# Performance work log

Hardware: AMD Instinct MI355X
Metric: run time of the kernel (lower is better)

The kernel has to match this reference:

```python
import jax, jax.numpy as jnp
import numpy as np

N_NODES = 50000
N_EDGES = 600000
N_GRAPHS = 64
IN_D, HID, EMB = 5, 128, 64
BN_EPS = 1e-5


def setup_inputs() -> dict:
    key = jax.random.key(0)
    ks = jax.random.split(key, 16)
    x = jax.random.normal(ks[0], (N_NODES, IN_D), dtype=jnp.float32)
    src = jax.random.randint(ks[1], (N_EDGES,), 0, N_NODES, dtype=jnp.int32)
    dst = jax.random.randint(ks[2], (N_EDGES,), 0, N_NODES, dtype=jnp.int32)
    batch = jnp.sort(jax.random.randint(ks[3], (N_NODES,), 0, N_GRAPHS, dtype=jnp.int32))
    def lin(k, fi, fo):
        s = 1.0 / np.sqrt(fi)
        kw, kb = jax.random.split(k)
        return (jax.random.uniform(kw, (fi, fo), jnp.float32, -s, s),
                jax.random.uniform(kb, (fo,), jnp.float32, -s, s))
    W1, b1 = lin(ks[4], IN_D, HID)
    W2, b2 = lin(ks[5], HID, HID)
    W3, b3 = lin(ks[6], HID, HID)
    Wp, bp = lin(ks[7], HID, EMB)
    g1 = 1.0 + 0.1 * jax.random.normal(ks[8], (HID,), jnp.float32)
    g2 = 1.0 + 0.1 * jax.random.normal(ks[9], (HID,), jnp.float32)
    g3 = 1.0 + 0.1 * jax.random.normal(ks[10], (HID,), jnp.float32)
    be1 = 0.1 * jax.random.normal(ks[11], (HID,), jnp.float32)
    be2 = 0.1 * jax.random.normal(ks[12], (HID,), jnp.float32)
    be3 = 0.1 * jax.random.normal(ks[13], (HID,), jnp.float32)
    return dict(x=x, src=src, dst=dst, batch=batch,
                W1=W1, b1=b1, W2=W2, b2=b2, W3=W3, b3=b3,
                g1=g1, be1=be1, g2=g2, be2=be2, g3=g3, be3=be3,
                Wp=Wp, bp=bp)


def reference(x, src, dst, batch, W1, b1, W2, b2, W3, b3,
              g1, be1, g2, be2, g3, be3, Wp, bp):
    n = x.shape[0]
    # GCNConv with self-loops and symmetric normalization (PyG default)
    loop = jnp.arange(n, dtype=src.dtype)
    s = jnp.concatenate([src, loop])
    d = jnp.concatenate([dst, loop])
    deg = jax.ops.segment_sum(jnp.ones_like(d, dtype=x.dtype), d, num_segments=n)
    dinv = jnp.where(deg > 0, jax.lax.rsqrt(deg), 0.0)
    norm = (dinv[s] * dinv[d])[:, None]  # (E+N, 1)

    def gcn(h, W, b):
        hw = h @ W                                   # (N, HID)
        msg = hw[s] * norm                           # gather + scale
        agg = jax.ops.segment_sum(msg, d, num_segments=n)
        return agg + b

    def bn_relu(h, g, be):
        # eval-mode BatchNorm1d with running_mean=0, running_var=1
        return jax.nn.relu(h * (g * jax.lax.rsqrt(jnp.asarray(1.0 + BN_EPS, h.dtype))) + be)

    h = bn_relu(gcn(x, W1, b1), g1, be1)
    h = bn_relu(gcn(h, W2, b2), g2, be2)
    h = bn_relu(gcn(h, W3, b3), g3, be3)

    # global mean pool over graphs
    sums = jax.ops.segment_sum(h, batch, num_segments=N_GRAPHS)
    cnt = jax.ops.segment_sum(jnp.ones((n,), h.dtype), batch, num_segments=N_GRAPHS)
    pooled = sums / jnp.maximum(cnt, 1.0)[:, None]
    return pooled @ Wp + bp
```

## Files before the change

kernel.cpp:

```cpp
#include <hip/hip_runtime.h>
#include <hip/hip_fp16.h>

#define N_NODES 50000
#define N_EDGES 600000
#define N_GRAPHS 64
#define IN_D 5
#define HID 128
#define EMB 64

#define CHUNK 512
#define NCHUNK ((N_NODES + CHUNK - 1) / CHUNK)
#define NREP 16
#define NLOC 4
#define TB 16

typedef _Float16 half8 __attribute__((ext_vector_type(8)));
typedef float float4v __attribute__((ext_vector_type(4)));
typedef float floatx2 __attribute__((ext_vector_type(2)));

__device__ __forceinline__ float ep_w(unsigned pe) {
    return (float)__ushort_as_half((unsigned short)(pe >> 16));
}
__device__ __forceinline__ unsigned ep_s(unsigned pe) { return pe & 0xffffu; }


__global__ __launch_bounds__(256) void k_init(int* __restrict__ cnt) {
    int tid = blockIdx.x * blockDim.x + threadIdx.x;
    if (tid < N_NODES) cnt[tid] = 0;
}


__global__ __launch_bounds__(256) void k_count(
        const int* __restrict__ dst, int* __restrict__ cnt,
        float* __restrict__ psum_rep,
        const float* __restrict__ W2, const float* __restrict__ W3,
        _Float16* __restrict__ Wt2, _Float16* __restrict__ Wt3,
        unsigned int* __restrict__ e_pack,
        const float* __restrict__ x, float* __restrict__ xp) {
    int tid = blockIdx.x * blockDim.x + threadIdx.x;
    int nt = gridDim.x * blockDim.x;
    if (tid < N_EDGES) atomicAdd(&cnt[dst[tid]], 1);
    if (tid < 8) e_pack[N_EDGES + tid] = 0u;
    for (int i = tid; i < NREP * N_GRAPHS * HID; i += nt) psum_rep[i] = 0.f;
    for (int i = tid; i < N_NODES * 8; i += nt) {
        int f = i & 7, n = i >> 3;
        xp[i] = (f < IN_D) ? x[n * IN_D + f] : 0.f;
    }
    for (int i = tid; i < 2 * HID * HID; i += nt) {
        int rem = i & (HID * HID - 1);
        int k = rem & 127, f = rem >> 7;
        if (i < HID * HID) Wt2[rem] = (_Float16)W2[k * HID + f];
        else               Wt3[rem] = (_Float16)W3[k * HID + f];
    }
}


__global__ void k_chunksum(const int* __restrict__ cnt, int* __restrict__ csum,
                           float* __restrict__ dinv) {
    __shared__ int sh[256];
    int b = blockIdx.x, t = threadIdx.x;
    int i0 = b * CHUNK + t, i1 = i0 + 256;
    int v = 0;
    if (i0 < N_NODES) { int c = cnt[i0]; v += c; dinv[i0] = rsqrtf((float)c + 1.0f); }
    if (i1 < N_NODES) { int c = cnt[i1]; v += c; dinv[i1] = rsqrtf((float)c + 1.0f); }
    sh[t] = v; __syncthreads();
    for (int off = 128; off > 0; off >>= 1) {
        if (t < off) sh[t] += sh[t + off];
        __syncthreads();
    }
    if (t == 0) csum[b] = sh[0];
}


__global__ void k_scan(const int* __restrict__ cnt, const int* __restrict__ csum,
                       int* __restrict__ row_start) {
    __shared__ int ws[4];
    int b = blockIdx.x, t = threadIdx.x;
    int lane = t & 63, w = t >> 6;

    int pre = 0;
    for (int j = lane; j < b; j += 64) pre += csum[j];
    #pragma unroll
    for (int off = 32; off > 0; off >>= 1) pre += __shfl_down(pre, off);
    pre = __shfl(pre, 0);

    int base = b * CHUNK;
    int i0 = base + 2 * t, i1 = i0 + 1;
    int c0 = (i0 < N_NODES) ? cnt[i0] : 0;
    int c1 = (i1 < N_NODES) ? cnt[i1] : 0;
    int v = c0 + c1;
    int s = v;
    #pragma unroll
    for (int off = 1; off < 64; off <<= 1) {
        int u = __shfl_up(s, off);
        if (lane >= off) s += u;
    }
    if (lane == 63) ws[w] = s;
    __syncthreads();
    if (t == 0) {
        int r = 0;
        #pragma unroll
        for (int j = 0; j < 4; ++j) { int xx = ws[j]; ws[j] = r; r += xx; }
    }
    __syncthreads();
    int excl = s - v + ws[w] + pre;
    if (i0 < N_NODES) row_start[i0] = excl;
    if (i1 < N_NODES) row_start[i1] = excl + c0;
    if (b == 0 && t == 0) row_start[N_NODES] = N_EDGES;
}


__global__ __launch_bounds__(256) void k_scatter(
        const int* __restrict__ src, const int* __restrict__ dst,
        const float* __restrict__ dinv, const int* __restrict__ row_start,
        int* __restrict__ cnt, unsigned int* __restrict__ e_pack) {
    int e = blockIdx.x * blockDim.x + threadIdx.x;
    if (e >= N_EDGES) return;
    int d = dst[e];
    int pos = row_start[d] + atomicSub(&cnt[d], 1) - 1;
    int s = src[e];
    unsigned hw = (unsigned)__half_as_ushort(__float2half(dinv[s]));
    e_pack[pos] = (hw << 16) | (unsigned)s;
}


__global__ __launch_bounds__(256) void k_agg1(
        const float* __restrict__ xp, const float* __restrict__ dinv,
        const int* __restrict__ row_start, const unsigned int* __restrict__ e_pack,
        const float* __restrict__ W1, const float* __restrict__ b1,
        const float* __restrict__ g1, const float* __restrict__ be1,
        unsigned short* __restrict__ H8u) {
    int t = threadIdx.x;
    int w = t >> 6, lane = t & 63;
    int slot8 = lane >> 3, q8 = lane & 7;
    int nb = blockIdx.x * TB;

    const float rs = rsqrtf(1.0f + 1e-5f);
    int fa = lane * 2, fb = fa + 1;
    float w1a[IN_D], w1b[IN_D];
    #pragma unroll
    for (int k = 0; k < IN_D; ++k) {
        w1a[k] = W1[k * HID + fa];
        w1b[k] = W1[k * HID + fb];
    }
    float b1a = b1[fa], b1b = b1[fb];
    float g1a = g1[fa] * rs, g1b = g1[fb] * rs;
    float e1a = be1[fa], e1b = be1[fb];

    #pragma unroll 1
    for (int i = 0; i < 2; ++i) {
        int n0 = nb + w * 4 + i * 2;
        int beg0 = row_start[n0], end0 = row_start[n0 + 1], end1 = row_start[n0 + 2];
        float acc0 = 0.f, acc1 = 0.f;
        int e0 = beg0, e1 = end0;
        while (e0 < end0 && e1 < end1) {
            unsigned pe0 = e_pack[e0 + slot8];
            unsigned pe1 = e_pack[e1 + slot8];
            float fw0 = (e0 + slot8 < end0) ? ep_w(pe0) : 0.f;
            float fw1 = (e1 + slot8 < end1) ? ep_w(pe1) : 0.f;
            float v0 = xp[(size_t)ep_s(pe0) * 8 + q8];
            float v1 = xp[(size_t)ep_s(pe1) * 8 + q8];
            acc0 = fmaf(fw0, v0, acc0);
            acc1 = fmaf(fw1, v1, acc1);
            e0 += 8; e1 += 8;
        }
        while (e0 < end0) {
            unsigned pe0 = e_pack[e0 + slot8];
            float fw0 = (e0 + slot8 < end0) ? ep_w(pe0) : 0.f;
            acc0 = fmaf(fw0, xp[(size_t)ep_s(pe0) * 8 + q8], acc0);
            e0 += 8;
        }
        while (e1 < end1) {
            unsigned pe1 = e_pack[e1 + slot8];
            float fw1 = (e1 + slot8 < end1) ? ep_w(pe1) : 0.f;
            acc1 = fmaf(fw1, xp[(size_t)ep_s(pe1) * 8 + q8], acc1);
            e1 += 8;
        }
        #pragma unroll
        for (int off = 8; off < 64; off <<= 1) {
            acc0 += __shfl_xor(acc0, off);
            acc1 += __shfl_xor(acc1, off);
        }
        #pragma unroll
        for (int p2 = 0; p2 < 2; ++p2) {
            int n = n0 + p2;
            float accs = p2 ? acc1 : acc0;
            float di = dinv[n];
            float av = di * fmaf(di, xp[(size_t)n * 8 + q8], accs);
            float a0 = __shfl(av, 0), a1 = __shfl(av, 1), a2 = __shfl(av, 2),
                  a3 = __shfl(av, 3), a4 = __shfl(av, 4);
            float va = b1a, vb = b1b;
            va = fmaf(a0, w1a[0], va); vb = fmaf(a0, w1b[0], vb);
            va = fmaf(a1, w1a[1], va); vb = fmaf(a1, w1b[1], vb);
            va = fmaf(a2, w1a[2], va); vb = fmaf(a2, w1b[2], vb);
            va = fmaf(a3, w1a[3], va); vb = fmaf(a3, w1b[3], vb);
            va = fmaf(a4, w1a[4], va); vb = fmaf(a4, w1b[4], vb);
            va = fmaf(va, g1a, e1a);
            vb = fmaf(vb, g1b, e1b);
            va = va > 0.f ? va : 0.f;
            vb = vb > 0.f ? vb : 0.f;
            int p = __builtin_amdgcn_cvt_pk_fp8_f32(va, vb, 0, false);
            H8u[(size_t)n * 64 + lane] = (unsigned short)(p & 0xffff);
        }
    }
}


__device__ __forceinline__ void acc_row_fp8(float* __restrict__ acc, float fw, uint4 g) {
    unsigned int gw[4] = {g.x, g.y, g.z, g.w};
    #pragma unroll
    for (int q = 0; q < 4; ++q) {
        floatx2 lo = __builtin_amdgcn_cvt_pk_f32_fp8(gw[q], false);
        floatx2 hi = __builtin_amdgcn_cvt_pk_f32_fp8(gw[q], true);
        acc[4 * q + 0] = fmaf(fw, lo[0], acc[4 * q + 0]);
        acc[4 * q + 1] = fmaf(fw, lo[1], acc[4 * q + 1]);
        acc[4 * q + 2] = fmaf(fw, hi[0], acc[4 * q + 2]);
        acc[4 * q + 3] = fmaf(fw, hi[1], acc[4 * q + 3]);
    }
}

__device__ __forceinline__ void agg_pair_fp8(
        const unsigned int* __restrict__ H8, const float* __restrict__ dinv,
        const int* __restrict__ row_start, const unsigned int* __restrict__ e_pack,
        int n0, int slot8, int q8,
        _Float16* __restrict__ row0, _Float16* __restrict__ row1) {
    float acc0[16], acc1[16];
    #pragma unroll
    for (int j = 0; j < 16; ++j) { acc0[j] = 0.f; acc1[j] = 0.f; }
    int beg0 = row_start[n0], end0 = row_start[n0 + 1], end1 = row_start[n0 + 2];
    int e0 = beg0, e1 = end0;
    while (e0 < end0 && e1 < end1) {
        unsigned pe0 = e_pack[e0 + slot8];
        unsigned pe1 = e_pack[e1 + slot8];
        float fw0 = (e0 + slot8 < end0) ? ep_w(pe0) : 0.f;
        float fw1 = (e1 + slot8 < end1) ? ep_w(pe1) : 0.f;
        uint4 g0 = ((const uint4*)(H8 + (size_t)ep_s(pe0) * 32))[q8];
        uint4 g1 = ((const uint4*)(H8 + (size_t)ep_s(pe1) * 32))[q8];
        acc_row_fp8(acc0, fw0, g0);
        acc_row_fp8(acc1, fw1, g1);
        e0 += 8; e1 += 8;
    }
    while (e0 < end0) {
        unsigned pe0 = e_pack[e0 + slot8];
        float fw0 = (e0 + slot8 < end0) ? ep_w(pe0) : 0.f;
        uint4 g0 = ((const uint4*)(H8 + (size_t)ep_s(pe0) * 32))[q8];
        acc_row_fp8(acc0, fw0, g0);
        e0 += 8;
    }
    while (e1 < end1) {
        unsigned pe1 = e_pack[e1 + slot8];
        float fw1 = (e1 + slot8 < end1) ? ep_w(pe1) : 0.f;
        uint4 g1 = ((const uint4*)(H8 + (size_t)ep_s(pe1) * 32))[q8];
        acc_row_fp8(acc1, fw1, g1);
        e1 += 8;
    }
    #pragma unroll
    for (int j = 0; j < 16; ++j) {
        float a = acc0[j];
        a += __shfl_xor(a, 8); a += __shfl_xor(a, 16); a += __shfl_xor(a, 32);
        acc0[j] = a;
        float b = acc1[j];
        b += __shfl_xor(b, 8); b += __shfl_xor(b, 16); b += __shfl_xor(b, 32);
        acc1[j] = b;
    }
    if (slot8 == 0) {
        float di0 = dinv[n0], di1 = dinv[n0 + 1];
        uint4 s0 = ((const uint4*)(H8 + (size_t)n0 * 32))[q8];
        uint4 s1 = ((const uint4*)(H8 + (size_t)(n0 + 1) * 32))[q8];
        unsigned int sw0[4] = {s0.x, s0.y, s0.z, s0.w};
        unsigned int sw1[4] = {s1.x, s1.y, s1.z, s1.w};
        half8 o0a, o0b, o1a, o1b;
        #pragma unroll
        for (int q = 0; q < 4; ++q) {
            floatx2 lo0 = __builtin_amdgcn_cvt_pk_f32_fp8(sw0[q], false);
            floatx2 hi0 = __builtin_amdgcn_cvt_pk_f32_fp8(sw0[q], true);
            floatx2 lo1 = __builtin_amdgcn_cvt_pk_f32_fp8(sw1[q], false);
            floatx2 hi1 = __builtin_amdgcn_cvt_pk_f32_fp8(sw1[q], true);
            int j = 4 * q;
            float f0[4] = {lo0[0], lo0[1], hi0[0], hi0[1]};
            float f1[4] = {lo1[0], lo1[1], hi1[0], hi1[1]};
            #pragma unroll
            for (int u = 0; u < 4; ++u) {
                float r0 = di0 * fmaf(di0, f0[u], acc0[j + u]);
                float r1 = di1 * fmaf(di1, f1[u], acc1[j + u]);
                if (j + u < 8) { o0a[j + u] = (_Float16)r0; o1a[j + u] = (_Float16)r1; }
                else           { o0b[j + u - 8] = (_Float16)r0; o1b[j + u - 8] = (_Float16)r1; }
            }
        }
        *(half8*)(row0 + q8 * 16)     = o0a;
        *(half8*)(row0 + q8 * 16 + 8) = o0b;
        *(half8*)(row1 + q8 * 16)     = o1a;
        *(half8*)(row1 + q8 * 16 + 8) = o1b;
    }
}


__global__ __launch_bounds__(256) void k_fuse2(
        const unsigned int* __restrict__ Hin, const float* __restrict__ dinv,
        const int* __restrict__ row_start, const unsigned int* __restrict__ e_pack,
        const _Float16* __restrict__ Wt,
        const float* __restrict__ bb, const float* __restrict__ gg,
        const float* __restrict__ bee, unsigned char* __restrict__ out8) {
    __shared__ __align__(16) _Float16 As[TB][136];
    int t = threadIdx.x;
    int w = t >> 6, lane = t & 63;
    int slot8 = lane >> 3, q8 = lane & 7;
    int nb = blockIdx.x * TB;

    #pragma unroll 1
    for (int i = 0; i < 2; ++i)
        agg_pair_fp8(Hin, dinv, row_start, e_pack, nb + w * 4 + i * 2,
                     slot8, q8, &As[w * 4 + i * 2][0], &As[w * 4 + i * 2 + 1][0]);
    __syncthreads();

    int quad = lane >> 4, r16 = lane & 15;
    half8 a[4];
    #pragma unroll
    for (int kb = 0; kb < 4; ++kb)
        a[kb] = *(const half8*)&As[r16][(kb * 4 + quad) * 8];
    const float rs = rsqrtf(1.0f + 1e-5f);
    #pragma unroll
    for (int fi = 0; fi < 2; ++fi) {
        int f = (w * 2 + fi) * 16 + r16;
        const half8* Brow = (const half8*)(Wt + (size_t)f * 128);
        float4v acc = {0.f, 0.f, 0.f, 0.f};
        #pragma unroll
        for (int kb = 0; kb < 4; ++kb)
            acc = __builtin_amdgcn_mfma_f32_16x16x32_f16(a[kb], Brow[kb * 4 + quad],
                                                         acc, 0, 0, 0);
        float b0 = bb[f], gf = gg[f] * rs, e0 = bee[f];
        #pragma unroll
        for (int rr = 0; rr < 4; ++rr) {
            float v = fmaf(acc[rr] + b0, gf, e0);
            v = v > 0.f ? v : 0.f;
            int p = __builtin_amdgcn_cvt_pk_fp8_f32(v, 0.f, 0, false);
            out8[(size_t)(nb + quad * 4 + rr) * 128 + f] = (unsigned char)(p & 0xff);
        }
    }
}


__global__ __launch_bounds__(256) void k_fuse3(
        const unsigned int* __restrict__ Hin, const float* __restrict__ dinv,
        const int* __restrict__ row_start, const unsigned int* __restrict__ e_pack,
        const _Float16* __restrict__ Wt,
        const float* __restrict__ bb, const float* __restrict__ gg,
        const float* __restrict__ bee, const int* __restrict__ batch,
        float* __restrict__ psum_rep) {
    __shared__ __align__(16) _Float16 As[TB][136];
    __shared__ float sh_pool[NLOC][HID];
    int t = threadIdx.x;
    int w = t >> 6, lane = t & 63;
    int slot8 = lane >> 3, q8 = lane & 7;
    int blk = (int)blockIdx.x;
    int nb = blk * TB;

    for (int i = t; i < NLOC * HID; i += 256) ((float*)sh_pool)[i] = 0.f;
    __syncthreads();

    #pragma unroll 1
    for (int i = 0; i < 2; ++i)
        agg_pair_fp8(Hin, dinv, row_start, e_pack, nb + w * 4 + i * 2,
                     slot8, q8, &As[w * 4 + i * 2][0], &As[w * 4 + i * 2 + 1][0]);

    int quad = lane >> 4, r16 = lane & 15;
    int g0 = batch[nb];
    int gi4[4];
    #pragma unroll
    for (int rr = 0; rr < 4; ++rr) gi4[rr] = batch[nb + quad * 4 + rr];
    __syncthreads();

    half8 a[4];
    #pragma unroll
    for (int kb = 0; kb < 4; ++kb)
        a[kb] = *(const half8*)&As[r16][(kb * 4 + quad) * 8];
    float* rep = psum_rep + (size_t)(blk & (NREP - 1)) * N_GRAPHS * HID;
    const float rs = rsqrtf(1.0f + 1e-5f);
    #pragma unroll
    for (int fi = 0; fi < 2; ++fi) {
        int f = (w * 2 + fi) * 16 + r16;
        const half8* Brow = (const half8*)(Wt + (size_t)f * 128);
        float4v acc = {0.f, 0.f, 0.f, 0.f};
        #pragma unroll
        for (int kb = 0; kb < 4; ++kb)
            acc = __builtin_amdgcn_mfma_f32_16x16x32_f16(a[kb], Brow[kb * 4 + quad],
                                                         acc, 0, 0, 0);
        float b0 = bb[f], gf = gg[f] * rs, e0 = bee[f];
        float partial = 0.f;
        int cur = -1;
        #pragma unroll
        for (int rr = 0; rr < 4; ++rr) {
            float v = fmaf(acc[rr] + b0, gf, e0);
            v = v > 0.f ? v : 0.f;
            int gi = gi4[rr];
            if (gi != cur) {
                if (cur >= 0) {
                    int idx = cur - g0;
                    if (idx < NLOC) atomicAdd(&sh_pool[idx][f], partial);
                    else            atomicAdd(&rep[cur * HID + f], partial);
                }
                partial = 0.f; cur = gi;
            }
            partial += v;
        }
        if (cur >= 0) {
            int idx = cur - g0;
            if (idx < NLOC) atomicAdd(&sh_pool[idx][f], partial);
            else            atomicAdd(&rep[cur * HID + f], partial);
        }
    }
    __syncthreads();
    for (int i = t; i < NLOC * HID; i += 256) {
        int idx = i >> 7, ff = i & 127;
        float v = sh_pool[idx][ff];
        int g = g0 + idx;
        if (v != 0.f && g < N_GRAPHS) atomicAdd(&rep[g * HID + ff], v);
    }
}


__device__ __forceinline__ int lower_bound_batch(const int* __restrict__ batch, int val) {
    int lo = 0, hi = N_NODES;
    while (lo < hi) {
        int mid = (lo + hi) >> 1;
        if (batch[mid] < val) lo = mid + 1;
        else hi = mid;
    }
    return lo;
}

__global__ void k_final(const float* __restrict__ psum_rep, const int* __restrict__ batch,
                        const float* __restrict__ Wp, const float* __restrict__ bp,
                        float* __restrict__ out) {
    __shared__ float s_p[HID];
    int gi = blockIdx.x, e = threadIdx.x;
    for (int f = e; f < HID; f += EMB) {
        float v = 0.f;
        #pragma unroll
        for (int r = 0; r < NREP; ++r)
            v += psum_rep[(size_t)r * N_GRAPHS * HID + gi * HID + f];
        s_p[f] = v;
    }
    int lane = e & 63;
    int r = 0;
    if (lane < 2) r = lower_bound_batch(batch, gi + lane);
    int c0 = __shfl(r, 0), c1 = __shfl(r, 1);
    float inv = 1.0f / fmaxf((float)(c1 - c0), 1.0f);
    __syncthreads();
    float acc = bp[e];
    #pragma unroll 8
    for (int f = 0; f < HID; ++f)
        acc = fmaf(s_p[f] * inv, Wp[f * EMB + e], acc);
    out[gi * EMB + e] = acc;
}


extern "C" void kernel_launch(void* const* d_in, const int* in_sizes, int n_in,
                              void* d_out, int out_size, void* d_ws, size_t ws_size,
                              hipStream_t stream) {
    const float* x   = (const float*)d_in[0];
    const int*   src = (const int*)d_in[1];
    const int*   dst = (const int*)d_in[2];
    const int* batch = (const int*)d_in[3];
    const float* W1 = (const float*)d_in[4];
    const float* b1 = (const float*)d_in[5];
    const float* W2 = (const float*)d_in[6];
    const float* b2 = (const float*)d_in[7];
    const float* W3 = (const float*)d_in[8];
    const float* b3 = (const float*)d_in[9];
    const float* g1 = (const float*)d_in[10];
    const float* be1 = (const float*)d_in[11];
    const float* g2 = (const float*)d_in[12];
    const float* be2 = (const float*)d_in[13];
    const float* g3 = (const float*)d_in[14];
    const float* be3 = (const float*)d_in[15];
    const float* Wp = (const float*)d_in[16];
    const float* bp = (const float*)d_in[17];
    float* out = (float*)d_out;

    char* ws = (char*)d_ws;
    size_t o = 0;
    auto alloc = [&](size_t bytes) {
        void* pp = ws + o;
        o += bytes;
        o = (o + 255) & ~255ull;
        return pp;
    };
    int*      cnt       = (int*)alloc(N_NODES * 4);
    int*      row_start = (int*)alloc((N_NODES + 1) * 4);
    int*      csum      = (int*)alloc(NCHUNK * 4);
    float*    dinv      = (float*)alloc(N_NODES * 4);
    unsigned int* e_pack = (unsigned int*)alloc((size_t)(N_EDGES + 8) * 4);
    _Float16* Wt2       = (_Float16*)alloc(HID * HID * 2);
    _Float16* Wt3       = (_Float16*)alloc(HID * HID * 2);
    float*    xp        = (float*)alloc((size_t)N_NODES * 8 * 4);
    unsigned int* H8a   = (unsigned int*)alloc((size_t)N_NODES * HID);
    unsigned int* H8b   = (unsigned int*)alloc((size_t)N_NODES * HID);
    float*    psum_rep  = (float*)alloc((size_t)NREP * N_GRAPHS * HID * 4);

    k_init<<<(N_NODES + 255) / 256, 256, 0, stream>>>(cnt);
    k_count<<<(N_EDGES + 255) / 256, 256, 0, stream>>>(dst, cnt, psum_rep,
                                                       W2, W3, Wt2, Wt3, e_pack, x, xp);
    k_chunksum<<<NCHUNK, 256, 0, stream>>>(cnt, csum, dinv);
    k_scan<<<NCHUNK, 256, 0, stream>>>(cnt, csum, row_start);
    k_scatter<<<(N_EDGES + 255) / 256, 256, 0, stream>>>(src, dst, dinv, row_start,
                                                         cnt, e_pack);
    k_agg1<<<N_NODES / TB, 256, 0, stream>>>(xp, dinv, row_start, e_pack,
                                             W1, b1, g1, be1, (unsigned short*)H8a);
    k_fuse2<<<N_NODES / TB, 256, 0, stream>>>(H8a, dinv, row_start, e_pack, Wt2,
                                              b2, g2, be2, (unsigned char*)H8b);
    k_fuse3<<<N_NODES / TB, 256, 0, stream>>>(H8b, dinv, row_start, e_pack, Wt3,
                                              b3, g3, be3, batch, psum_rep);
    k_final<<<N_GRAPHS, EMB, 0, stream>>>(psum_rep, batch, Wp, bp, out);
}
```

Baseline: 262.5 us.

## Split fp8 feature matrix into column halves and aggregate each half separately

Stores the fp8 hidden features as two column-half planes (64 features each) instead of row-major 128-byte rows. A new kernel aggregates the first half into an fp16 buffer, and the fused layer kernel aggregates the second half before running the MFMA transform. The aim is to halve the gather working set per pass so it fits better in cache for the random neighbour gathers. In exchange it adds two kernel launches, an extra fp16 intermediate buffer, and a second full pass over the edge list per layer.

```diff
diff --git a/kernel.cpp b/kernel.cpp
--- a/kernel.cpp
+++ b/kernel.cpp
@@ -146,6 +146,7 @@
     float b1a = b1[fa], b1b = b1[fb];
     float g1a = g1[fa] * rs, g1b = g1[fb] * rs;
     float e1a = be1[fa], e1b = be1[fb];
+    size_t outbase = (size_t)(lane >> 5) * N_NODES * 32 + (lane & 31);
 
     #pragma unroll 1
     for (int i = 0; i < 2; ++i) {
@@ -200,105 +201,80 @@
             va = va > 0.f ? va : 0.f;
             vb = vb > 0.f ? vb : 0.f;
             int p = __builtin_amdgcn_cvt_pk_fp8_f32(va, vb, 0, false);
-            H8u[(size_t)n * 64 + lane] = (unsigned short)(p & 0xffff);
-        }
-    }
-}
-
-
-__device__ __forceinline__ void acc_row_fp8(float* __restrict__ acc, float fw, uint4 g) {
-    unsigned int gw[4] = {g.x, g.y, g.z, g.w};
-    #pragma unroll
-    for (int q = 0; q < 4; ++q) {
-        floatx2 lo = __builtin_amdgcn_cvt_pk_f32_fp8(gw[q], false);
-        floatx2 hi = __builtin_amdgcn_cvt_pk_f32_fp8(gw[q], true);
-        acc[4 * q + 0] = fmaf(fw, lo[0], acc[4 * q + 0]);
-        acc[4 * q + 1] = fmaf(fw, lo[1], acc[4 * q + 1]);
-        acc[4 * q + 2] = fmaf(fw, hi[0], acc[4 * q + 2]);
-        acc[4 * q + 3] = fmaf(fw, hi[1], acc[4 * q + 3]);
-    }
-}
-
-__device__ __forceinline__ void agg_pair_fp8(
+            H8u[outbase + (size_t)n * 32] = (unsigned short)(p & 0xffff);
+        }
+    }
+}
+
+
+__device__ __forceinline__ void agg_half(
+        const uint2* __restrict__ P, float di, int beg, int end,
+        const unsigned int* __restrict__ e_pack,
+        int n, int slot8, int q8, _Float16* __restrict__ rowdst) {
+    float acc[8];
+    #pragma unroll
+    for (int j = 0; j < 8; ++j) acc[j] = 0.f;
+    for (int e = beg; e < end; e += 8) {
+        unsigned pe = e_pack[e + slot8];
+        float fw = (e + slot8 < end) ? ep_w(pe) : 0.f;
+        uint2 g = P[(size_t)ep_s(pe) * 8 + q8];
+        floatx2 l0 = __builtin_amdgcn_cvt_pk_f32_fp8(g.x, false);
+        floatx2 h0 = __builtin_amdgcn_cvt_pk_f32_fp8(g.x, true);
+        floatx2 l1 = __builtin_amdgcn_cvt_pk_f32_fp8(g.y, false);
+        floatx2 h1 = __builtin_amdgcn_cvt_pk_f32_fp8(g.y, true);
+        acc[0] = fmaf(fw, l0[0], acc[0]);
+        acc[1] = fmaf(fw, l0[1], acc[1]);
+        acc[2] = fmaf(fw, h0[0], acc[2]);
+        acc[3] = fmaf(fw, h0[1], acc[3]);
+        acc[4] = fmaf(fw, l1[0], acc[4]);
+        acc[5] = fmaf(fw, l1[1], acc[5]);
+        acc[6] = fmaf(fw, h1[0], acc[6]);
+        acc[7] = fmaf(fw, h1[1], acc[7]);
+    }
+    #pragma unroll
+    for (int j = 0; j < 8; ++j) {
+        float a = acc[j];
+        a += __shfl_xor(a, 8); a += __shfl_xor(a, 16); a += __shfl_xor(a, 32);
+        acc[j] = a;
+    }
+    if (slot8 == 0) {
+        uint2 s = P[(size_t)n * 8 + q8];
+        floatx2 l0 = __builtin_amdgcn_cvt_pk_f32_fp8(s.x, false);
+        floatx2 h0 = __builtin_amdgcn_cvt_pk_f32_fp8(s.x, true);
+        floatx2 l1 = __builtin_amdgcn_cvt_pk_f32_fp8(s.y, false);
+        floatx2 h1 = __builtin_amdgcn_cvt_pk_f32_fp8(s.y, true);
+        float sv[8] = {l0[0], l0[1], h0[0], h0[1], l1[0], l1[1], h1[0], h1[1]};
+        half8 o;
+        #pragma unroll
+        for (int j = 0; j < 8; ++j)
+            o[j] = (_Float16)(di * fmaf(di, sv[j], acc[j]));
+        *(half8*)(rowdst + q8 * 8) = o;
+    }
+}
+
+
+__global__ __launch_bounds__(256) void k_fuseA(
         const unsigned int* __restrict__ H8, const float* __restrict__ dinv,
         const int* __restrict__ row_start, const unsigned int* __restrict__ e_pack,
-        int n0, int slot8, int q8,
-        _Float16* __restrict__ row0, _Float16* __restrict__ row1) {
-    float acc0[16], acc1[16];
-    #pragma unroll
-    for (int j = 0; j < 16; ++j) { acc0[j] = 0.f; acc1[j] = 0.f; }
-    int beg0 = row_start[n0], end0 = row_start[n0 + 1], end1 = row_start[n0 + 2];
-    int e0 = beg0, e1 = end0;
-    while (e0 < end0 && e1 < end1) {
-        unsigned pe0 = e_pack[e0 + slot8];
-        unsigned pe1 = e_pack[e1 + slot8];
-        float fw0 = (e0 + slot8 < end0) ? ep_w(pe0) : 0.f;
-        float fw1 = (e1 + slot8 < end1) ? ep_w(pe1) : 0.f;
-        uint4 g0 = ((const uint4*)(H8 + (size_t)ep_s(pe0) * 32))[q8];
-        uint4 g1 = ((const uint4*)(H8 + (size_t)ep_s(pe1) * 32))[q8];
-        acc_row_fp8(acc0, fw0, g0);
-        acc_row_fp8(acc1, fw1, g1);
-        e0 += 8; e1 += 8;
-    }
-    while (e0 < end0) {
-        unsigned pe0 = e_pack[e0 + slot8];
-        float fw0 = (e0 + slot8 < end0) ? ep_w(pe0) : 0.f;
-        uint4 g0 = ((const uint4*)(H8 + (size_t)ep_s(pe0) * 32))[q8];
-        acc_row_fp8(acc0, fw0, g0);
-        e0 += 8;
-    }
-    while (e1 < end1) {
-        unsigned pe1 = e_pack[e1 + slot8];
-        float fw1 = (e1 + slot8 < end1) ? ep_w(pe1) : 0.f;
-        uint4 g1 = ((const uint4*)(H8 + (size_t)ep_s(pe1) * 32))[q8];
-        acc_row_fp8(acc1, fw1, g1);
-        e1 += 8;
-    }
-    #pragma unroll
-    for (int j = 0; j < 16; ++j) {
-        float a = acc0[j];
-        a += __shfl_xor(a, 8); a += __shfl_xor(a, 16); a += __shfl_xor(a, 32);
-        acc0[j] = a;
-        float b = acc1[j];
-        b += __shfl_xor(b, 8); b += __shfl_xor(b, 16); b += __shfl_xor(b, 32);
-        acc1[j] = b;
-    }
-    if (slot8 == 0) {
-        float di0 = dinv[n0], di1 = dinv[n0 + 1];
-        uint4 s0 = ((const uint4*)(H8 + (size_t)n0 * 32))[q8];
-        uint4 s1 = ((const uint4*)(H8 + (size_t)(n0 + 1) * 32))[q8];
-        unsigned int sw0[4] = {s0.x, s0.y, s0.z, s0.w};
-        unsigned int sw1[4] = {s1.x, s1.y, s1.z, s1.w};
-        half8 o0a, o0b, o1a, o1b;
-        #pragma unroll
-        for (int q = 0; q < 4; ++q) {
-            floatx2 lo0 = __builtin_amdgcn_cvt_pk_f32_fp8(sw0[q], false);
-            floatx2 hi0 = __builtin_amdgcn_cvt_pk_f32_fp8(sw0[q], true);
-            floatx2 lo1 = __builtin_amdgcn_cvt_pk_f32_fp8(sw1[q], false);
-            floatx2 hi1 = __builtin_amdgcn_cvt_pk_f32_fp8(sw1[q], true);
-            int j = 4 * q;
-            float f0[4] = {lo0[0], lo0[1], hi0[0], hi0[1]};
-            float f1[4] = {lo1[0], lo1[1], hi1[0], hi1[1]};
-            #pragma unroll
-            for (int u = 0; u < 4; ++u) {
-                float r0 = di0 * fmaf(di0, f0[u], acc0[j + u]);
-                float r1 = di1 * fmaf(di1, f1[u], acc1[j + u]);
-                if (j + u < 8) { o0a[j + u] = (_Float16)r0; o1a[j + u] = (_Float16)r1; }
-                else           { o0b[j + u - 8] = (_Float16)r0; o1b[j + u - 8] = (_Float16)r1; }
-            }
-        }
-        *(half8*)(row0 + q8 * 16)     = o0a;
-        *(half8*)(row0 + q8 * 16 + 8) = o0b;
-        *(half8*)(row1 + q8 * 16)     = o1a;
-        *(half8*)(row1 + q8 * 16 + 8) = o1b;
-    }
-}
-
-
-__global__ __launch_bounds__(256) void k_fuse2(
-        const unsigned int* __restrict__ Hin, const float* __restrict__ dinv,
-        const int* __restrict__ row_start, const unsigned int* __restrict__ e_pack,
-        const _Float16* __restrict__ Wt,
+        _Float16* __restrict__ Ah) {
+    int t = threadIdx.x;
+    int w = t >> 6, lane = t & 63;
+    int slot8 = lane >> 3, q8 = lane & 7;
+    int nb = blockIdx.x * TB;
+    const uint2* P = (const uint2*)H8;
+    #pragma unroll 1
+    for (int i = 0; i < 4; ++i) {
+        int n = nb + w * 4 + i;
+        agg_half(P, dinv[n], row_start[n], row_start[n + 1], e_pack,
+                 n, slot8, q8, Ah + (size_t)n * 64);
+    }
+}
+
+
+__global__ __launch_bounds__(256) void k_fuse2b(
+        const unsigned int* __restrict__ H8, const _Float16* __restrict__ Ah,
+        const float* __restrict__ dinv, const int* __restrict__ row_start,
+        const unsigned int* __restrict__ e_pack, const _Float16* __restrict__ Wt,
         const float* __restrict__ bb, const float* __restrict__ gg,
         const float* __restrict__ bee, unsigned char* __restrict__ out8) {
     __shared__ __align__(16) _Float16 As[TB][136];
@@ -307,10 +283,18 @@
     int slot8 = lane >> 3, q8 = lane & 7;
     int nb = blockIdx.x * TB;
 
+    {
+        const uint2* srcp = (const uint2*)(Ah + (size_t)nb * 64);
+        uint2 v = srcp[t];
+        *(uint2*)&As[t >> 4][(t & 15) * 4] = v;
+    }
+    const uint2* P1 = (const uint2*)(H8 + (size_t)N_NODES * 16);
     #pragma unroll 1
-    for (int i = 0; i < 2; ++i)
-        agg_pair_fp8(Hin, dinv, row_start, e_pack, nb + w * 4 + i * 2,
-                     slot8, q8, &As[w * 4 + i * 2][0], &As[w * 4 + i * 2 + 1][0]);
+    for (int i = 0; i < 4; ++i) {
+        int n = nb + w * 4 + i;
+        agg_half(P1, dinv[n], row_start[n], row_start[n + 1], e_pack,
+                 n, slot8, q8, &As[w * 4 + i][64]);
+    }
     __syncthreads();
 
     int quad = lane >> 4, r16 = lane & 15;
@@ -329,21 +313,22 @@
             acc = __builtin_amdgcn_mfma_f32_16x16x32_f16(a[kb], Brow[kb * 4 + quad],
                                                          acc, 0, 0, 0);
         float b0 = bb[f], gf = gg[f] * rs, e0 = bee[f];
+        size_t pbase = (size_t)(f >> 6) * N_NODES * 64 + (f & 63);
         #pragma unroll
         for (int rr = 0; rr < 4; ++rr) {
             float v = fmaf(acc[rr] + b0, gf, e0);
             v = v > 0.f ? v : 0.f;
             int p = __builtin_amdgcn_cvt_pk_fp8_f32(v, 0.f, 0, false);
-            out8[(size_t)(nb + quad * 4 + rr) * 128 + f] = (unsigned char)(p & 0xff);
-        }
-    }
-}
-
-
-__global__ __launch_bounds__(256) void k_fuse3(
-        const unsigned int* __restrict__ Hin, const float* __restrict__ dinv,
-        const int* __restrict__ row_start, const unsigned int* __restrict__ e_pack,
-        const _Float16* __restrict__ Wt,
+            out8[pbase + (size_t)(nb + quad * 4 + rr) * 64] = (unsigned char)(p & 0xff);
+        }
+    }
+}
+
+
+__global__ __launch_bounds__(256) void k_fuse3b(
+        const unsigned int* __restrict__ H8, const _Float16* __restrict__ Ah,
+        const float* __restrict__ dinv, const int* __restrict__ row_start,
+        const unsigned int* __restrict__ e_pack, const _Float16* __restrict__ Wt,
         const float* __restrict__ bb, const float* __restrict__ gg,
         const float* __restrict__ bee, const int* __restrict__ batch,
         float* __restrict__ psum_rep) {
@@ -356,12 +341,18 @@
     int nb = blk * TB;
 
     for (int i = t; i < NLOC * HID; i += 256) ((float*)sh_pool)[i] = 0.f;
-    __syncthreads();
-
+    {
+        const uint2* srcp = (const uint2*)(Ah + (size_t)nb * 64);
+        uint2 v = srcp[t];
+        *(uint2*)&As[t >> 4][(t & 15) * 4] = v;
+    }
+    const uint2* P1 = (const uint2*)(H8 + (size_t)N_NODES * 16);
     #pragma unroll 1
-    for (int i = 0; i < 2; ++i)
-        agg_pair_fp8(Hin, dinv, row_start, e_pack, nb + w * 4 + i * 2,
-                     slot8, q8, &As[w * 4 + i * 2][0], &As[w * 4 + i * 2 + 1][0]);
+    for (int i = 0; i < 4; ++i) {
+        int n = nb + w * 4 + i;
+        agg_half(P1, dinv[n], row_start[n], row_start[n + 1], e_pack,
+                 n, slot8, q8, &As[w * 4 + i][64]);
+    }
 
     int quad = lane >> 4, r16 = lane & 15;
     int g0 = batch[nb];
@@ -496,6 +487,7 @@
     float*    xp        = (float*)alloc((size_t)N_NODES * 8 * 4);
     unsigned int* H8a   = (unsigned int*)alloc((size_t)N_NODES * HID);
     unsigned int* H8b   = (unsigned int*)alloc((size_t)N_NODES * HID);
+    _Float16* Ah        = (_Float16*)alloc((size_t)N_NODES * 64 * 2);
     float*    psum_rep  = (float*)alloc((size_t)NREP * N_GRAPHS * HID * 4);
 
     k_init<<<(N_NODES + 255) / 256, 256, 0, stream>>>(cnt);
@@ -507,9 +499,11 @@
                                                          cnt, e_pack);
     k_agg1<<<N_NODES / TB, 256, 0, stream>>>(xp, dinv, row_start, e_pack,
                                              W1, b1, g1, be1, (unsigned short*)H8a);
-    k_fuse2<<<N_NODES / TB, 256, 0, stream>>>(H8a, dinv, row_start, e_pack, Wt2,
-                                              b2, g2, be2, (unsigned char*)H8b);
-    k_fuse3<<<N_NODES / TB, 256, 0, stream>>>(H8b, dinv, row_start, e_pack, Wt3,
-                                              b3, g3, be3, batch, psum_rep);
+    k_fuseA<<<N_NODES / TB, 256, 0, stream>>>(H8a, dinv, row_start, e_pack, Ah);
+    k_fuse2b<<<N_NODES / TB, 256, 0, stream>>>(H8a, Ah, dinv, row_start, e_pack, Wt2,
+                                               b2, g2, be2, (unsigned char*)H8b);
+    k_fuseA<<<N_NODES / TB, 256, 0, stream>>>(H8b, dinv, row_start, e_pack, Ah);
+    k_fuse3b<<<N_NODES / TB, 256, 0, stream>>>(H8b, Ah, dinv, row_start, e_pack, Wt3,
+                                               b3, g3, be3, batch, psum_rep);
     k_final<<<N_GRAPHS, EMB, 0, stream>>>(psum_rep, batch, Wp, bp, out);
 }
```

Result: slower. 286.8 us (+9.2%).
